# Kernel optimization log

Hardware: AMD Instinct MI355X
Metric: run time of the kernel (lower is better)

Reference implementation:

```python
import jax, jax.numpy as jnp
import numpy as np

D_LOW = 32
LAGS = [1, 2, 4, 8]
# Upper-triangular pair indices (offset=1), matching torch.triu_indices(d_low, d_low, 1)
IDX_I, IDX_J = np.triu_indices(D_LOW, k=1)
IDX_I = jnp.asarray(IDX_I)
IDX_J = jnp.asarray(IDX_J)
EPS = 1e-6


def setup_inputs() -> dict:
    key = jax.random.key(0)
    ks = jax.random.split(key, 7)
    b, n, d_model = 4, 4096, 1024
    d_plucker = D_LOW * (D_LOW - 1) // 2  # 496
    s = lambda fan_in: 1.0 / np.sqrt(fan_in)
    return {
        "x": jax.random.normal(ks[0], (b, n, d_model), dtype=jnp.float32),
        "W_red": jax.random.normal(ks[1], (d_model, D_LOW), dtype=jnp.float32) * s(d_model),
        "b_red": jax.random.normal(ks[2], (D_LOW,), dtype=jnp.float32) * s(d_model),
        "W_exp": jax.random.normal(ks[3], (d_plucker, d_model), dtype=jnp.float32) * s(d_plucker),
        "b_exp": jax.random.normal(ks[4], (d_model,), dtype=jnp.float32) * s(d_plucker),
        "W_gate": jax.random.normal(ks[5], (2 * d_model, d_model), dtype=jnp.float32) * s(2 * d_model),
        "b_gate": jax.random.normal(ks[6], (d_model,), dtype=jnp.float32) * s(2 * d_model),
    }


def reference(x, W_red, b_red, W_exp, b_exp, W_gate, b_gate):
    b, n, _ = x.shape
    d_plucker = D_LOW * (D_LOW - 1) // 2
    z = x @ W_red + b_red  # [b, n, d_low]
    plucker_total = jnp.zeros((b, n, d_plucker), dtype=x.dtype)
    counts = jnp.zeros((b, n, 1), dtype=x.dtype)
    for lag in LAGS:
        if lag <= 0 or lag >= n:
            continue
        z_curr = z[:, lag:, :]   # [b, n-lag, d_low]
        z_past = z[:, :-lag, :]  # [b, n-lag, d_low]
        # Antisymmetric Plucker coordinates over upper-triangular index pairs
        p = (z_curr[:, :, IDX_I] * z_past[:, :, IDX_J]
             - z_curr[:, :, IDX_J] * z_past[:, :, IDX_I])  # [b, n-lag, d_plucker]
        norm = jnp.linalg.norm(p, axis=-1, keepdims=True)
        p = p / jnp.maximum(norm, EPS)
        plucker_total = plucker_total.at[:, lag:, :].add(p)
        counts = counts.at[:, lag:, :].add(1.0)
    counts = jnp.maximum(counts, 1.0)
    plucker_avg = plucker_total / counts
    g_avg = plucker_avg @ W_exp + b_exp  # [b, n, d_model]
    concat = jnp.concatenate([x, g_avg], axis=-1)  # [b, n, 2*d_model]
    gate = jax.nn.sigmoid(concat @ W_gate + b_gate)
    return gate * x + (1.0 - gate) * g_avg
```

## Files before the change

### kernel.cpp

```cpp
#include <hip/hip_runtime.h>
#include <hip/hip_bf16.h>
#include <math.h>

#define B_DIM   4
#define N_DIM   4096
#define D_MODEL 1024
#define D_LOW   32
#define NPAIR   496
#define NROWS   (B_DIM * N_DIM)
#define KPAD3   512
#define LDA2    1536

typedef __bf16 bf16;
typedef __bf16 bf16x8 __attribute__((ext_vector_type(8)));
typedef __bf16 bf16x4 __attribute__((ext_vector_type(4)));
typedef float  f32x4  __attribute__((ext_vector_type(4)));

#define GLOAD_LDS16(g, l) __builtin_amdgcn_global_load_lds( \
    (__attribute__((address_space(1))) void*)(g),           \
    (__attribute__((address_space(3))) void*)(l), 16, 0, 0)

__global__ __launch_bounds__(256) void wred_t(const float* __restrict__ Wr,
                                              bf16* __restrict__ WrT) {
    __shared__ float tile[32][33];
    const int t  = threadIdx.x;
    const int kb = blockIdx.x * 32;
    {
        int k = t >> 3, c4 = (t & 7) * 4;
        float4 v = *reinterpret_cast<const float4*>(&Wr[(size_t)(kb + k) * 32 + c4]);
        tile[k][c4 + 0] = v.x; tile[k][c4 + 1] = v.y;
        tile[k][c4 + 2] = v.z; tile[k][c4 + 3] = v.w;
    }
    __syncthreads();
    {
        int c = t >> 3, kq = (t & 7) * 4;
        bf16x4 o = { (bf16)tile[kq + 0][c], (bf16)tile[kq + 1][c],
                     (bf16)tile[kq + 2][c], (bf16)tile[kq + 3][c] };
        *reinterpret_cast<bf16x4*>(&WrT[(size_t)c * 1024 + kb + kq]) = o;
    }
}

__global__ __launch_bounds__(256) void k1_mfma(const float* __restrict__ x,
                                               const bf16* __restrict__ WrT,
                                               bf16* __restrict__ a2,
                                               float* __restrict__ zpart) {
    const int t    = threadIdx.x;
    const int wv   = t >> 6, lane = t & 63;
    const int l15  = lane & 15, lhi = lane >> 4;
    const int kc   = blockIdx.x;
    const int mt   = blockIdx.y;
    const int row  = mt * 64 + wv * 16 + l15;
    const int kb   = kc * 256;

    f32x4 accz[2] = { (f32x4){0.f,0.f,0.f,0.f}, (f32x4){0.f,0.f,0.f,0.f} };

#pragma unroll
    for (int ks = 0; ks < 8; ++ks) {
        const int k0 = kb + ks * 32 + lhi * 8;
        const float4 u0 = *reinterpret_cast<const float4*>(&x[(size_t)row * 1024 + k0]);
        const float4 u1 = *reinterpret_cast<const float4*>(&x[(size_t)row * 1024 + k0 + 4]);
        bf16x8 af = { (bf16)u0.x, (bf16)u0.y, (bf16)u0.z, (bf16)u0.w,
                      (bf16)u1.x, (bf16)u1.y, (bf16)u1.z, (bf16)u1.w };
        *reinterpret_cast<bf16x8*>(&a2[(size_t)row * LDA2 + k0]) = af;
        const bf16x8 b0 = *reinterpret_cast<const bf16x8*>(
            &WrT[(size_t)l15 * 1024 + kb + ks * 32 + lhi * 8]);
        const bf16x8 b1 = *reinterpret_cast<const bf16x8*>(
            &WrT[(size_t)(16 + l15) * 1024 + kb + ks * 32 + lhi * 8]);
        accz[0] = __builtin_amdgcn_mfma_f32_16x16x32_bf16(af, b0, accz[0], 0, 0, 0);
        accz[1] = __builtin_amdgcn_mfma_f32_16x16x32_bf16(af, b1, accz[1], 0, 0, 0);
    }
#pragma unroll
    for (int cg = 0; cg < 2; ++cg)
#pragma unroll
        for (int r = 0; r < 4; ++r) {
            const int rout = mt * 64 + wv * 16 + lhi * 4 + r;
            zpart[((size_t)kc * NROWS + rout) * 32 + cg * 16 + l15] = accz[cg][r];
        }
}

__global__ __launch_bounds__(256) void k2_plucker(const float* __restrict__ zpart,
                                                  const float* __restrict__ br,
                                                  bf16* __restrict__ a2) {
    const int wv   = threadIdx.x >> 6;
    const int lane = threadIdx.x & 63;
    const int row  = blockIdx.x * 4 + wv;
    const int t    = row & (N_DIM - 1);
    const int c    = lane & 31;
    const float bias = br[c];

    float zc = bias;
#pragma unroll
    for (int p = 0; p < 4; ++p)
        zc += zpart[((size_t)p * NROWS + row) * 32 + c];

    float zp[4];
    float red[9];
    red[0] = zc * zc;
#pragma unroll
    for (int li = 0; li < 4; ++li) {
        const int lag = 1 << li;
        float v = 0.f;
        if (t >= lag) {
            v = bias;
#pragma unroll
            for (int p = 0; p < 4; ++p)
                v += zpart[((size_t)p * NROWS + (row - lag)) * 32 + c];
        }
        zp[li] = v;
        red[1 + li] = zc * zp[li];
        red[5 + li] = zp[li] * zp[li];
    }
#pragma unroll
    for (int m = 1; m < 32; m <<= 1) {
#pragma unroll
        for (int i = 0; i < 9; ++i) red[i] += __shfl_xor(red[i], m);
    }
    float cnt = 0.f;
#pragma unroll
    for (int li = 0; li < 4; ++li) cnt += (t >= (1 << li)) ? 1.f : 0.f;
    const float inv = 1.f / fmaxf(cnt, 1.f);

    float w = 0.f;
#pragma unroll
    for (int li = 0; li < 4; ++li) {
        float n2 = fmaxf(red[0] * red[5 + li] - red[1 + li] * red[1 + li], 0.f);
        float nr = sqrtf(n2);
        float s  = (t >= (1 << li)) ? inv / fmaxf(nr, 1e-6f) : 0.f;
        w += s * zp[li];
    }

#pragma unroll
    for (int u = 0; u < 8; ++u) {
        const int k = u * 64 + lane;
        float v = 0.f;
        if (k < NPAIR) {
            int kk = k, i = 0;
            while (kk >= 31 - i) { kk -= 31 - i; ++i; }
            const int j = i + 1 + kk;
            float zci = __shfl(zc, i), zcj = __shfl(zc, j);
            float wi  = __shfl(w, i),  wj  = __shfl(w, j);
            v = zci * wj - zcj * wi;
        }
        a2[(size_t)row * LDA2 + 1024 + k] = (bf16)v;
    }
}

__global__ __launch_bounds__(256) void transpose_cvt(const float* __restrict__ src,
                                                     bf16* __restrict__ dst,
                                                     int Ksrc, int Kpad) {
    __shared__ float tile[32][36];
    const int t  = threadIdx.x;
    const int kb = blockIdx.x * 32;
    const int nb = blockIdx.y * 32;
    int li = t * 4;
    int kl = li >> 5, nl = li & 31;
    float4 v = {0.f, 0.f, 0.f, 0.f};
    if (kb + kl < Ksrc)
        v = *reinterpret_cast<const float4*>(&src[(size_t)(kb + kl) * 1024 + nb + nl]);
    tile[kl][nl + 0] = v.x; tile[kl][nl + 1] = v.y;
    tile[kl][nl + 2] = v.z; tile[kl][nl + 3] = v.w;
    __syncthreads();
    int nl2 = li >> 5, kl2 = li & 31;
    bf16x4 o = { (bf16)tile[kl2 + 0][nl2], (bf16)tile[kl2 + 1][nl2],
                 (bf16)tile[kl2 + 2][nl2], (bf16)tile[kl2 + 3][nl2] };
    *reinterpret_cast<bf16x4*>(&dst[(size_t)(nb + nl2) * Kpad + kb + kl2]) = o;
}

__global__ __launch_bounds__(256) void we_cvt_be(const float* __restrict__ We,
                                                 const float* __restrict__ be,
                                                 bf16* __restrict__ WeB) {
    size_t o = ((size_t)blockIdx.x * 256 + threadIdx.x) * 4;
    int row = (int)(o >> 10), col = (int)(o & 1023);
    float4 v = {0.f, 0.f, 0.f, 0.f};
    if (row < NPAIR)      v = *reinterpret_cast<const float4*>(&We[(size_t)row * 1024 + col]);
    else if (row == NPAIR) v = *reinterpret_cast<const float4*>(&be[col]);
    bf16x4 b = { (bf16)v.x, (bf16)v.y, (bf16)v.z, (bf16)v.w };
    *reinterpret_cast<bf16x4*>(&WeB[o]) = b;
}

__global__ __launch_bounds__(256) void wcomb_mfma(const bf16* __restrict__ A,
                                                  const bf16* __restrict__ Bt,
                                                  bf16* __restrict__ BcT) {
    __shared__ bf16 As[128 * 32];
    __shared__ bf16 Bs[128 * 32];
    const int t    = threadIdx.x;
    const int mb   = blockIdx.y * 128;
    const int nbq  = blockIdx.x * 128;
    const int w    = t >> 6, lane = t & 63;
    const int wr   = w >> 1, wc = w & 1;
    const int l15  = lane & 15, lhi = lane >> 4;

    f32x4 acc[4][4];
#pragma unroll
    for (int mt = 0; mt < 4; ++mt)
#pragma unroll
        for (int nt = 0; nt < 4; ++nt) acc[mt][nt] = (f32x4){0.f, 0.f, 0.f, 0.f};

    const int li0 = t, li1 = t + 256;
    const int r0 = li0 >> 2, c0 = (li0 & 3) * 8;
    const int r1 = li1 >> 2, c1 = (li1 & 3) * 8;

    for (int kb = 0; kb < 1024; kb += 32) {
        GLOAD_LDS16(A  + (size_t)(mb + r0) * 1024 + kb + c0, As + li0 * 8);
        GLOAD_LDS16(A  + (size_t)(mb + r1) * 1024 + kb + c1, As + li1 * 8);
        GLOAD_LDS16(Bt + (size_t)(nbq + r0) * 1024 + kb + c0, Bs + li0 * 8);
        GLOAD_LDS16(Bt + (size_t)(nbq + r1) * 1024 + kb + c1, Bs + li1 * 8);
        __syncthreads();
        bf16x8 a[4], b[4];
#pragma unroll
        for (int mt = 0; mt < 4; ++mt)
            a[mt] = *reinterpret_cast<const bf16x8*>(
                As + (wr * 64 + mt * 16 + l15) * 32 + lhi * 8);
#pragma unroll
        for (int nt = 0; nt < 4; ++nt)
            b[nt] = *reinterpret_cast<const bf16x8*>(
                Bs + (wc * 64 + nt * 16 + l15) * 32 + lhi * 8);
#pragma unroll
        for (int mt = 0; mt < 4; ++mt)
#pragma unroll
            for (int nt = 0; nt < 4; ++nt)
                acc[mt][nt] = __builtin_amdgcn_mfma_f32_16x16x32_bf16(
                    a[mt], b[nt], acc[mt][nt], 0, 0, 0);
        __syncthreads();
    }
#pragma unroll
    for (int mt = 0; mt < 4; ++mt)
#pragma unroll
        for (int nt = 0; nt < 4; ++nt) {
            const int col = nbq + wc * 64 + nt * 16 + l15;
#pragma unroll
            for (int r = 0; r < 4; ++r) {
                const int row = mb + wr * 64 + mt * 16 + lhi * 4 + r;
                BcT[(size_t)row * 1536 + 1024 + col] = (bf16)acc[mt][nt][r];
            }
        }
}

__global__ __launch_bounds__(256) void bgc_extract(const float* __restrict__ bg,
                                                   const bf16* __restrict__ BcT,
                                                   float* __restrict__ bgc) {
    int n = blockIdx.x * 256 + threadIdx.x;
    bgc[n] = bg[n] + (float)BcT[(size_t)n * 1536 + 1024 + NPAIR];
}

template <int KDIM, int LDAp, int LDBp, bool GATE>
__global__ __launch_bounds__(512, 2) void gemm8p(const bf16* __restrict__ A,
                                                 const bf16* __restrict__ Bt,
                                                 const float* __restrict__ bias,
                                                 const bf16* __restrict__ gsrc,
                                                 bf16* __restrict__ gdst,
                                                 float* __restrict__ out) {
    extern __shared__ char lds[];
    const int t    = threadIdx.x;
    const int w    = t >> 6, lane = t & 63;
    const int wr   = w >> 2, wc = w & 3;
    const int l15  = lane & 15, lhi = lane >> 4;

    const int fid = blockIdx.x;
    const int xcd = fid & 7, loc = fid >> 3;
    const int mb  = (xcd * 8 + (loc >> 2)) * 256;
    const int nb  = (loc & 3) * 256;

    const int srow = t >> 3;
    const int scol = ((t & 7) ^ (srow & 7)) * 8;
    const size_t aOff = (size_t)(mb + srow) * LDAp + scol;
    const size_t bOff = (size_t)(nb + srow) * LDBp + scol;
    char* const ldsA = lds;
    char* const ldsB = lds + 65536;

#define STAGE_A(d, h, kb) do { \
    GLOAD_LDS16(A + aOff + (size_t)((h) * 128) * LDAp + (kb),      ldsA + (d) * 32768 + (h) * 16384 + t * 16); \
    GLOAD_LDS16(A + aOff + (size_t)((h) * 128 + 64) * LDAp + (kb), ldsA + (d) * 32768 + (h) * 16384 + 8192 + t * 16); } while (0)
#define STAGE_B(d, h, kb) do { \
    GLOAD_LDS16(Bt + bOff + (size_t)((h) * 128) * LDBp + (kb),      ldsB + (d) * 32768 + (h) * 16384 + t * 16); \
    GLOAD_LDS16(Bt + bOff + (size_t)((h) * 128 + 64) * LDBp + (kb), ldsB + (d) * 32768 + (h) * 16384 + 8192 + t * 16); } while (0)

    const int swx = (l15 & 7) << 4;
#define LDAF(d, mq_) do { const char* Ab_ = ldsA + (d) * 32768 + wr * 16384; \
    _Pragma("unroll") for (int mf = 0; mf < 4; ++mf) \
    _Pragma("unroll") for (int ks = 0; ks < 2; ++ks) { \
        int lin = ((mq_) * 64 + mf * 16 + l15) * 128 + ks * 64 + lhi * 16; \
        afr[mf][ks] = *reinterpret_cast<const bf16x8*>(Ab_ + (lin ^ swx)); } } while (0)
#define LDBF(d, nq_) do { const char* Bb_ = ldsB + (d) * 32768 + (wc >> 1) * 16384; \
    _Pragma("unroll") for (int nf = 0; nf < 2; ++nf) \
    _Pragma("unroll") for (int ks = 0; ks < 2; ++ks) { \
        int lin = ((wc & 1) * 64 + (nq_) * 32 + nf * 16 + l15) * 128 + ks * 64 + lhi * 16; \
        bfr[nf][ks] = *reinterpret_cast<const bf16x8*>(Bb_ + (lin ^ swx)); } } while (0)
#define MMA(mq_, nq_) do { __builtin_amdgcn_s_setprio(1); \
    _Pragma("unroll") for (int mf = 0; mf < 4; ++mf) \
    _Pragma("unroll") for (int nf = 0; nf < 2; ++nf) \
    _Pragma("unroll") for (int ks = 0; ks < 2; ++ks) \
        acc[(mq_) * 4 + mf][(nq_) * 2 + nf] = __builtin_amdgcn_mfma_f32_16x16x32_bf16( \
            afr[mf][ks], bfr[nf][ks], acc[(mq_) * 4 + mf][(nq_) * 2 + nf], 0, 0, 0); \
    __builtin_amdgcn_s_setprio(0); } while (0)
#define BAR() asm volatile("s_barrier" ::: "memory")

    f32x4 acc[8][4];
#pragma unroll
    for (int i = 0; i < 8; ++i)
#pragma unroll
        for (int j = 0; j < 4; ++j) acc[i][j] = (f32x4){0.f, 0.f, 0.f, 0.f};
    bf16x8 afr[4][2], bfr[2][2];

    STAGE_B(0, 0, 0); STAGE_B(0, 1, 0);
    STAGE_A(0, 0, 0); STAGE_A(0, 1, 0);
    STAGE_B(1, 0, 64);
    asm volatile("s_waitcnt vmcnt(2)" ::: "memory");
    BAR();

    const int NT    = KDIM / 64;
    const int ITERS = NT / 2;
    for (int it = 0; it < ITERS; ++it) {
        const int k1e = (it * 2 + 1) * 64;
        const int k2e = (it * 2 + 2) * 64;
        const int k3e = (it * 2 + 3) * 64;
        const bool s2 = (it * 2 + 2) < NT;
        const bool s3 = (it * 2 + 3) < NT;
        const bool lastit = (it == ITERS - 1);

        STAGE_B(1, 1, k1e); STAGE_A(1, 0, k1e);
        LDAF(0, 0); LDBF(0, 0);
        BAR(); MMA(0, 0); BAR();
        STAGE_A(1, 1, k1e);
        LDAF(0, 1);
        BAR(); MMA(1, 0); BAR();
        LDBF(0, 1);
        BAR(); MMA(1, 1); BAR();
        if (s2) STAGE_B(0, 0, k2e);
        LDAF(0, 0);
        BAR(); MMA(0, 1);
        if (lastit) asm volatile("s_waitcnt vmcnt(0)" ::: "memory");
        else        asm volatile("s_waitcnt vmcnt(2)" ::: "memory");
        BAR();

        if (s2) { STAGE_B(0, 1, k2e); STAGE_A(0, 0, k2e); }
        LDAF(1, 0); LDBF(1, 0);
        BAR(); MMA(0, 0); BAR();
        if (s2) STAGE_A(0, 1, k2e);
        LDAF(1, 1);
        BAR(); MMA(1, 0); BAR();
        LDBF(1, 1);
        BAR(); MMA(1, 1); BAR();
        if (s3) STAGE_B(1, 0, k3e);
        LDAF(1, 0);
        BAR(); MMA(0, 1);
        if (lastit) asm volatile("s_waitcnt vmcnt(0)" ::: "memory");
        else        asm volatile("s_waitcnt vmcnt(2)" ::: "memory");
        BAR();
    }
#undef STAGE_A
#undef STAGE_B
#undef LDAF
#undef LDBF
#undef MMA
#undef BAR

#pragma unroll
    for (int mi = 0; mi < 8; ++mi) {
#pragma unroll
        for (int nf = 0; nf < 4; ++nf) {
            const int col = nb + wc * 64 + nf * 16 + l15;
            const float bv = bias[col];
#pragma unroll
            for (int r = 0; r < 4; ++r) {
                const int row = mb + wr * 128 + mi * 16 + lhi * 4 + r;
                float v = acc[mi][nf][r] + bv;
                if constexpr (GATE) {
                    float gate = 1.f / (1.f + expf(-v));
                    float xv = (float)A[(size_t)row * LDAp + col];
                    float gv = (float)gsrc[(size_t)row * D_MODEL + col];
                    out[(size_t)row * D_MODEL + col] = gate * xv + (1.f - gate) * gv;
                } else {
                    gdst[(size_t)row * D_MODEL + col] = (bf16)v;
                }
            }
        }
    }
}

extern "C" void kernel_launch(void* const* d_in, const int* in_sizes, int n_in,
                              void* d_out, int out_size, void* d_ws, size_t ws_size,
                              hipStream_t stream) {
    const float* x  = (const float*)d_in[0];
    const float* Wr = (const float*)d_in[1];
    const float* br = (const float*)d_in[2];
    const float* We = (const float*)d_in[3];
    const float* be = (const float*)d_in[4];
    const float* Wg = (const float*)d_in[5];
    const float* bg = (const float*)d_in[6];
    float* out = (float*)d_out;

    char* ws = (char*)d_ws;
    bf16*  gbuf  = (bf16*)(ws);
    float* zpart = (float*)(ws);
    bf16*  A2    = (bf16*)(ws + (32u << 20));
    bf16*  WeT   = (bf16*)(ws + (80u << 20));
    bf16*  BcT   = (bf16*)(ws + (81u << 20));
    bf16*  WgbT  = (bf16*)(ws + (84u << 20));
    bf16*  WeB   = (bf16*)(ws + (86u << 20));
    float* bgc   = (float*)(ws + (87u << 20));
    bf16*  WrT   = (bf16*)(ws + (88u << 20));

    (void)hipFuncSetAttribute(reinterpret_cast<const void*>(&gemm8p<KPAD3, LDA2, KPAD3, false>),
                              hipFuncAttributeMaxDynamicSharedMemorySize, 131072);
    (void)hipFuncSetAttribute(reinterpret_cast<const void*>(&gemm8p<1536, LDA2, 1536, true>),
                              hipFuncAttributeMaxDynamicSharedMemorySize, 131072);

    wred_t<<<32, 256, 0, stream>>>(Wr, WrT);
    k1_mfma<<<dim3(4, 256), 256, 0, stream>>>(x, WrT, A2, zpart);
    k2_plucker<<<NROWS / 4, 256, 0, stream>>>(zpart, br, A2);

    transpose_cvt<<<dim3(KPAD3 / 32, 1024 / 32), 256, 0, stream>>>(We, WeT, NPAIR, KPAD3);
    transpose_cvt<<<dim3(1024 / 32, 1024 / 32), 256, 0, stream>>>(Wg, BcT, 1024, 1536);
    transpose_cvt<<<dim3(1024 / 32, 1024 / 32), 256, 0, stream>>>(Wg + (size_t)1024 * 1024, WgbT, 1024, 1024);
    we_cvt_be<<<512, 256, 0, stream>>>(We, be, WeB);
    wcomb_mfma<<<dim3(4, 8), 256, 0, stream>>>(WgbT, WeB, BcT);
    bgc_extract<<<4, 256, 0, stream>>>(bg, BcT, bgc);

    gemm8p<KPAD3, LDA2, KPAD3, false><<<256, 512, 131072, stream>>>(
        A2 + 1024, WeT, be, nullptr, gbuf, nullptr);
    gemm8p<1536, LDA2, 1536, true><<<256, 512, 131072, stream>>>(
        A2, BcT, bgc, gbuf, nullptr, out);
}
```

Before: 171.8 us.

## Double-buffer MFMA register fragments to overlap LDS reads with MMA

Splits the A/B register fragments into two sets, so LDS fragment loads for the next sub-tile are issued while MFMAs consume the current set. This removes about half the barriers in the main loop. Launch bounds drop from 2 to 1 block per CU to make room for the extra registers, which lowers occupancy. There is also a risk of reading LDS stages before their async loads have fully landed, because a fragment load now runs after the final loop iteration.

```diff
diff --git a/kernel.cpp b/kernel.cpp
--- a/kernel.cpp
+++ b/kernel.cpp
@@ -244,7 +244,7 @@
 }
 
 template <int KDIM, int LDAp, int LDBp, bool GATE>
-__global__ __launch_bounds__(512, 2) void gemm8p(const bf16* __restrict__ A,
+__global__ __launch_bounds__(512, 1) void gemm8p(const bf16* __restrict__ A,
                                                  const bf16* __restrict__ Bt,
                                                  const float* __restrict__ bias,
                                                  const bf16* __restrict__ gsrc,
@@ -276,22 +276,22 @@
     GLOAD_LDS16(Bt + bOff + (size_t)((h) * 128 + 64) * LDBp + (kb), ldsB + (d) * 32768 + (h) * 16384 + 8192 + t * 16); } while (0)
 
     const int swx = (l15 & 7) << 4;
-#define LDAF(d, mq_) do { const char* Ab_ = ldsA + (d) * 32768 + wr * 16384; \
+#define LDAF(dst, d, mq_) do { const char* Ab_ = ldsA + (d) * 32768 + wr * 16384; \
     _Pragma("unroll") for (int mf = 0; mf < 4; ++mf) \
     _Pragma("unroll") for (int ks = 0; ks < 2; ++ks) { \
         int lin = ((mq_) * 64 + mf * 16 + l15) * 128 + ks * 64 + lhi * 16; \
-        afr[mf][ks] = *reinterpret_cast<const bf16x8*>(Ab_ + (lin ^ swx)); } } while (0)
-#define LDBF(d, nq_) do { const char* Bb_ = ldsB + (d) * 32768 + (wc >> 1) * 16384; \
+        dst[mf][ks] = *reinterpret_cast<const bf16x8*>(Ab_ + (lin ^ swx)); } } while (0)
+#define LDBF(dst, d, nq_) do { const char* Bb_ = ldsB + (d) * 32768 + (wc >> 1) * 16384; \
     _Pragma("unroll") for (int nf = 0; nf < 2; ++nf) \
     _Pragma("unroll") for (int ks = 0; ks < 2; ++ks) { \
         int lin = ((wc & 1) * 64 + (nq_) * 32 + nf * 16 + l15) * 128 + ks * 64 + lhi * 16; \
-        bfr[nf][ks] = *reinterpret_cast<const bf16x8*>(Bb_ + (lin ^ swx)); } } while (0)
-#define MMA(mq_, nq_) do { __builtin_amdgcn_s_setprio(1); \
+        dst[nf][ks] = *reinterpret_cast<const bf16x8*>(Bb_ + (lin ^ swx)); } } while (0)
+#define MMA(aset, bset, mq_, nq_) do { __builtin_amdgcn_s_setprio(1); \
     _Pragma("unroll") for (int mf = 0; mf < 4; ++mf) \
     _Pragma("unroll") for (int nf = 0; nf < 2; ++nf) \
     _Pragma("unroll") for (int ks = 0; ks < 2; ++ks) \
         acc[(mq_) * 4 + mf][(nq_) * 2 + nf] = __builtin_amdgcn_mfma_f32_16x16x32_bf16( \
-            afr[mf][ks], bfr[nf][ks], acc[(mq_) * 4 + mf][(nq_) * 2 + nf], 0, 0, 0); \
+            aset[mf][ks], bset[nf][ks], acc[(mq_) * 4 + mf][(nq_) * 2 + nf], 0, 0, 0); \
     __builtin_amdgcn_s_setprio(0); } while (0)
 #define BAR() asm volatile("s_barrier" ::: "memory")
 
@@ -300,13 +300,14 @@
     for (int i = 0; i < 8; ++i)
 #pragma unroll
         for (int j = 0; j < 4; ++j) acc[i][j] = (f32x4){0.f, 0.f, 0.f, 0.f};
-    bf16x8 afr[4][2], bfr[2][2];
+    bf16x8 afrA[4][2], afrB[4][2], bfrA[2][2], bfrB[2][2];
 
     STAGE_B(0, 0, 0); STAGE_B(0, 1, 0);
     STAGE_A(0, 0, 0); STAGE_A(0, 1, 0);
     STAGE_B(1, 0, 64);
     asm volatile("s_waitcnt vmcnt(2)" ::: "memory");
     BAR();
+    LDAF(afrA, 0, 0); LDBF(bfrA, 0, 0);
 
     const int NT    = KDIM / 64;
     const int ITERS = NT / 2;
@@ -319,33 +320,39 @@
         const bool lastit = (it == ITERS - 1);
 
         STAGE_B(1, 1, k1e); STAGE_A(1, 0, k1e);
-        LDAF(0, 0); LDBF(0, 0);
-        BAR(); MMA(0, 0); BAR();
+        LDAF(afrB, 0, 1);
+        MMA(afrA, bfrA, 0, 0);
+        BAR();
         STAGE_A(1, 1, k1e);
-        LDAF(0, 1);
-        BAR(); MMA(1, 0); BAR();
-        LDBF(0, 1);
-        BAR(); MMA(1, 1); BAR();
+        LDBF(bfrB, 0, 1);
+        MMA(afrB, bfrA, 1, 0);
+        BAR();
+        MMA(afrB, bfrB, 1, 1);
+        BAR();
         if (s2) STAGE_B(0, 0, k2e);
-        LDAF(0, 0);
-        BAR(); MMA(0, 1);
         if (lastit) asm volatile("s_waitcnt vmcnt(0)" ::: "memory");
         else        asm volatile("s_waitcnt vmcnt(2)" ::: "memory");
         BAR();
+        LDAF(afrB, 1, 0); LDBF(bfrA, 1, 0);
+        MMA(afrA, bfrB, 0, 1);
+        BAR();
 
         if (s2) { STAGE_B(0, 1, k2e); STAGE_A(0, 0, k2e); }
-        LDAF(1, 0); LDBF(1, 0);
-        BAR(); MMA(0, 0); BAR();
+        LDAF(afrA, 1, 1);
+        MMA(afrB, bfrA, 0, 0);
+        BAR();
         if (s2) STAGE_A(0, 1, k2e);
-        LDAF(1, 1);
-        BAR(); MMA(1, 0); BAR();
-        LDBF(1, 1);
-        BAR(); MMA(1, 1); BAR();
+        LDBF(bfrB, 1, 1);
+        MMA(afrA, bfrA, 1, 0);
+        BAR();
+        MMA(afrA, bfrB, 1, 1);
+        BAR();
         if (s3) STAGE_B(1, 0, k3e);
-        LDAF(1, 0);
-        BAR(); MMA(0, 1);
         if (lastit) asm volatile("s_waitcnt vmcnt(0)" ::: "memory");
         else        asm volatile("s_waitcnt vmcnt(2)" ::: "memory");
+        BAR();
+        LDAF(afrA, 0, 0); LDBF(bfrA, 0, 0);
+        MMA(afrB, bfrB, 0, 1);
         BAR();
     }
 #undef STAGE_A
```

Result: slower. 257.2 us (+49.7%).
